# Optimization experiments

Measured on AMD Instinct MI355X. Metric: run time of the kernel, lower is better.

## Reference

```python
import jax, jax.numpy as jnp
import numpy as np

B, L, T = 32, 100, 50
V_SENT, V_FIELD, V_POS = 20000, 1500, 31
E_S, E_F, E_P = 400, 50, 5
FREP = E_F + 2 * E_P            # field rep = field + ppos + pneg embeds
H_DEC = 500                      # decoder hidden
H_DIR = H_DEC // 2               # per-direction encoder hidden
H_ENC = 500                      # encoder_hidden_size (attention/output dim)
IN_ENC = E_S + FREP
EPS = 1e-3


def lstm_cell(x, h, c, Wih, Whh, b):
    z = x @ Wih.T + h @ Whh.T + b
    i, f, g, o = jnp.split(z, 4, axis=-1)
    c = jax.nn.sigmoid(f) * c + jax.nn.sigmoid(i) * jnp.tanh(g)
    h = jax.nn.sigmoid(o) * jnp.tanh(c)
    return h, c


def setup_inputs():
    key = jax.random.key(0)
    ks = jax.random.split(key, 30)
    n = lambda k, sh, s=0.05: jax.random.normal(k, sh, jnp.float32) * s
    return {
        "value_mask": jnp.ones((B, L), jnp.float32),
        "align_prob": jax.random.uniform(ks[0], (B, L, V_SENT), jnp.float32),
        "E_sent": n(ks[1], (V_SENT, E_S)),
        "E_field": n(ks[2], (V_FIELD, E_F)),
        "E_ppos": n(ks[3], (V_POS, E_P)),
        "E_pneg": n(ks[4], (V_POS, E_P)),
        "E_target": n(ks[5], (V_SENT, 300)),
        "enc_Wih_f": n(ks[6], (4 * H_DIR, IN_ENC)),
        "enc_Whh_f": n(ks[7], (4 * H_DIR, H_DIR)),
        "enc_b_f": jnp.zeros((4 * H_DIR,), jnp.float32),
        "enc_Wih_b": n(ks[8], (4 * H_DIR, IN_ENC)),
        "enc_Whh_b": n(ks[9], (4 * H_DIR, H_DIR)),
        "enc_b_b": jnp.zeros((4 * H_DIR,), jnp.float32),
        "dec_Wih": n(ks[10], (4 * H_DEC, E_S)),
        "dec_Whh": n(ks[11], (4 * H_DEC, H_DEC)),
        "dec_b": jnp.zeros((4 * H_DEC,), jnp.float32),
        "W_d": n(ks[12], (H_DEC, H_ENC)),
        "W_z": n(ks[13], (H_DEC, FREP)),
        "W_out": n(ks[14], (H_DEC + H_ENC, H_ENC)),
        "b_out": jnp.zeros((H_ENC,), jnp.float32),
        "w_l": n(ks[15], (H_DEC + H_ENC + E_S, 1)),
        "b_l": jnp.zeros((1,), jnp.float32),
        "W_lin": n(ks[16], (V_SENT, H_ENC)),
        "b_lin": jnp.zeros((V_SENT,), jnp.float32),
        "sent": jax.random.randint(ks[17], (B, T), 0, V_SENT),
        "value": jax.random.randint(ks[18], (B, L), 0, V_SENT),
        "field": jax.random.randint(ks[19], (B, L), 0, V_FIELD),
        "ppos": jax.random.randint(ks[20], (B, L), 0, V_POS),
        "pneg": jax.random.randint(ks[21], (B, L), 0, V_POS),
        "batch_size": B,
    }


def _forward(value_mask, align_prob, E_sent, E_field, E_ppos, E_pneg, E_target,
             enc_Wih_f, enc_Whh_f, enc_b_f, enc_Wih_b, enc_Whh_b, enc_b_b,
             dec_Wih, dec_Whh, dec_b, W_d, W_z, W_out, b_out, w_l, b_l,
             W_lin, b_lin, sent, value, field, ppos, pneg):
    bsz = value.shape[0]
    inp_d = E_sent[value]                                             # [B,L,E_S]
    inp_z = jnp.concatenate([E_field[field], E_ppos[ppos], E_pneg[pneg]], axis=-1)  # [B,L,FREP]
    x = jnp.concatenate([inp_d, inp_z], axis=-1)                      # [B,L,IN_ENC]
    xs = jnp.transpose(x, (1, 0, 2))                                  # [L,B,IN_ENC]
    h0 = jnp.zeros((bsz, H_DIR), x.dtype)

    def enc_step(Wih, Whh, b):
        def f(carry, xt):
            h, c = lstm_cell(xt, carry[0], carry[1], Wih, Whh, b)
            return (h, c), h
        return f

    (hf, cf), hs_f = jax.lax.scan(enc_step(enc_Wih_f, enc_Whh_f, enc_b_f), (h0, h0), xs)
    (hb, cb), hs_b = jax.lax.scan(enc_step(enc_Wih_b, enc_Whh_b, enc_b_b), (h0, h0), xs[::-1])
    enc_out = jnp.transpose(jnp.concatenate([hs_f, hs_b[::-1]], axis=-1), (1, 0, 2))  # [B,L,H_ENC]
    # replicate torch .view on h_n [2,B,H_DIR] -> [B, 2*H_DIR] (row-major, as in source)
    h0_dec = jnp.stack([hf, hb]).reshape(bsz, 2 * H_DIR)
    c0_dec = jnp.stack([cf, cb]).reshape(bsz, 2 * H_DIR)

    sent_emb = jnp.transpose(E_sent[sent], (1, 0, 2))                 # [T,B,E_S]

    def dec_step(carry, xt):
        h, c = lstm_cell(xt, carry[0], carry[1], dec_Wih, dec_Whh, dec_b)
        s_d = jnp.einsum('be,ble->bl', h @ W_d, enc_out)              # attn over encoder states
        s_z = jnp.einsum('bf,blf->bl', h @ W_z, inp_z)                # attn over field reps
        a = jax.nn.softmax(s_d, axis=-1) * jax.nn.softmax(s_z, axis=-1)
        a = a / (jnp.sum(a, axis=-1, keepdims=True) + EPS)            # dual attention
        ctx = jnp.einsum('bl,ble->be', a, enc_out)
        hc = jnp.concatenate([h, ctx], axis=-1)
        out_t = jnp.tanh(hc @ W_out + b_out)                          # [B,H_ENC]
        lam_t = jax.nn.sigmoid(jnp.concatenate([hc, xt], axis=-1) @ w_l + b_l)  # [B,1]
        return (h, c), (out_t, a, lam_t)

    (hT, cT), (outs, attn, lam) = jax.lax.scan(dec_step, (h0_dec, c0_dec), sent_emb)
    outs = jnp.transpose(outs, (1, 0, 2))                             # [B,T,H_ENC]
    attn = jnp.transpose(attn, (1, 0, 2))                             # [B,T,L]
    lam = jnp.transpose(lam, (1, 0, 2))                               # [B,T,1]

    p_mod = jax.nn.log_softmax(outs @ W_lin.T + b_lin, axis=-1)       # [B,T,V]
    p_lex = jnp.einsum('btl,blv->btv', attn, align_prob)              # copy/lexical dist
    p_bias = jax.nn.log_softmax(lam * p_lex + (1.0 - lam) * p_mod, axis=-1)

    # vectorized replacement of the python double-loop position_idx_to_value
    max_idx = jnp.argmax(attn, axis=-1)                               # [B,T]
    word_idx = jnp.take_along_axis(value, max_idx, axis=1)            # [B,T]
    attn_pred = E_target[word_idx]                                    # [B,T,300]
    decoder_pred = E_target[jnp.argmax(p_bias, axis=-1)]              # [B,T,300]
    return p_bias, (hT, cT), attn_pred, decoder_pred


def reference(value_mask, align_prob, E_sent, E_field, E_ppos, E_pneg, E_target,
              enc_Wih_f, enc_Whh_f, enc_b_f, enc_Wih_b, enc_Whh_b, enc_b_b,
              dec_Wih, dec_Whh, dec_b, W_d, W_z, W_out, b_out, w_l, b_l,
              W_lin, b_lin, sent, value, field, ppos, pneg, batch_size):
    return _forward(value_mask, align_prob, E_sent, E_field, E_ppos, E_pneg, E_target,
                    enc_Wih_f, enc_Whh_f, enc_b_f, enc_Wih_b, enc_Whh_b, enc_b_b,
                    dec_Wih, dec_Whh, dec_b, W_d, W_z, W_out, b_out, w_l, b_l,
                    W_lin, b_lin, sent, value, field, ppos, pneg)
```

## Files before the change

kernel.cpp:

```cpp
#include <hip/hip_runtime.h>

#define DI __device__ __forceinline__

constexpr int B = 32, L = 100, T = 50;
constexpr int VS = 20000;
constexpr int HR = 250, HD = 500;
constexpr int INE = 460;
constexpr int OC = 1072;

constexpr size_t O_X      = 0;
constexpr size_t O_SX     = 5888000;
constexpr size_t O_WIHFT  = 8448000;
constexpr size_t O_WIHBT  = 10288000;
constexpr size_t O_WDECT  = 12128000;
constexpr size_t O_W4ENC  = 15328000;
constexpr size_t O_W4DEC  = 17328000;
constexpr size_t O_WCAT   = 21328000;
constexpr size_t O_XWF    = 23472000;
constexpr size_t O_XWB    = 49072000;
constexpr size_t O_XWD    = 74672000;
constexpr size_t O_EOB    = 100272000;
constexpr size_t O_E2     = 113072000;
constexpr size_t O_PROJ   = 125872000;
constexpr size_t O_EHB    = O_PROJ;
constexpr size_t O_DHB    = O_PROJ + 131072;
constexpr size_t O_HD     = 139593600;
constexpr size_t O_H0DEC  = 146249600;
constexpr size_t O_HENCF  = 146505600;
constexpr size_t O_CENCF  = 146633600;
constexpr size_t O_CDEC0  = 146761600;
constexpr size_t O_HDECF  = 146889600;
constexpr size_t O_CDECF  = 147017600;
constexpr size_t O_AD     = 147145600;
constexpr size_t O_ATTN   = 148425600;
constexpr size_t O_EWL    = 149065600;
constexpr size_t O_SXL    = 149091200;
constexpr size_t O_AWL    = 149104000;
constexpr size_t O_LAM    = 149116800;
constexpr size_t O_LS1    = 149123200;
constexpr size_t O_WIDX   = 149129600;
constexpr size_t O_OUTS   = 149144192;
constexpr size_t O_FLG    = 154090496;

constexpr size_t OUT_HT  = 32000000;
constexpr size_t OUT_CT  = 32016000;
constexpr size_t OUT_AP  = 32032000;
constexpr size_t OUT_DP  = 32512000;

DI double dsig(double x) { return 1.0 / (1.0 + exp(-x)); }

DI double cld(const double* p) {
    return __hip_atomic_load(p, __ATOMIC_RELAXED, __HIP_MEMORY_SCOPE_AGENT);
}
DI void cst(double* p, double v) {
    __hip_atomic_store(p, v, __ATOMIC_RELAXED, __HIP_MEMORY_SCOPE_AGENT);
}
DI int cldi(const int* p) {
    return __hip_atomic_load(p, __ATOMIC_RELAXED, __HIP_MEMORY_SCOPE_AGENT);
}
DI void csti(int* p, int v) {
    __hip_atomic_store(p, v, __ATOMIC_RELAXED, __HIP_MEMORY_SCOPE_AGENT);
}
DI void spinge(const int* p, int target) {
    int spins = 0;
    while (cldi(p) < target) {
        __builtin_amdgcn_s_sleep(1);
        if (++spins > 50000000) break;
    }
}


__global__ void k_embed_x(const float* Es, const float* Ef, const float* Ep, const float* En,
                          const int* value, const int* field, const int* ppos, const int* pneg,
                          float* x) {
    int i = blockIdx.x * 256 + threadIdx.x;
    if (i >= B * L * INE) return;
    int j = i % INE, bl = i / INE;
    float v;
    if (j < 400)      v = Es[(size_t)value[bl] * 400 + j];
    else if (j < 450) v = Ef[(size_t)field[bl] * 50 + (j - 400)];
    else if (j < 455) v = Ep[(size_t)ppos[bl] * 5 + (j - 450)];
    else              v = En[(size_t)pneg[bl] * 5 + (j - 455)];
    x[i] = v;
}

__global__ void k_embed_sent(const float* Es, const int* sent, float* sx) {
    int i = blockIdx.x * 256 + threadIdx.x;
    if (i >= T * B * 400) return;
    int k = i % 400, tb = i / 400;
    int b = tb % B, t = tb / B;
    sx[i] = Es[(size_t)sent[b * T + t] * 400 + k];
}

__global__ void k_transpose(float* dst, const float* src, int K, int G) {
    int i = blockIdx.x * 256 + threadIdx.x;
    if (i >= K * G) return;
    int g = i % G, k = i / G;
    dst[i] = src[(size_t)g * K + k];
}

__global__ void k_pack4T(float* dst, const float* src, int U, int Kh) {
    int i = blockIdx.x * 256 + threadIdx.x;
    if (i >= U * Kh * 4) return;
    int g = i & 3, rest = i >> 2;
    int u = rest % U, k = rest / U;
    dst[i] = src[((size_t)(g * U + u)) * Kh + k];
}

__global__ void k_pack_wcat(float* dst, const float* Wd, const float* Wz, const float* Wo, const float* wl) {
    int i = blockIdx.x * 256 + threadIdx.x;
    if (i >= 500 * OC) return;
    int o = i % OC, d = i / OC;
    float v = 0.f;
    if (o < 500)       v = Wd[(size_t)d * 500 + o];
    else if (o < 560)  v = Wz[(size_t)d * 60 + (o - 500)];
    else if (o < 1060) v = Wo[(size_t)d * 500 + (o - 560)];
    else if (o == 1060) v = wl[d];
    dst[i] = v;
}

__global__ void k_zeroi(int* p, int n) {
    int i = blockIdx.x * 256 + threadIdx.x;
    if (i < n) p[i] = 0;
}

__global__ __launch_bounds__(256) void k_gemm_xw(double* out, const float* xs, int bstride, int tstride,
                                                 const float* Wt, const float* bias, int K, int G) {
    __shared__ float xls[460 * 33];
    int t = blockIdx.x;
    int g = blockIdx.y * 256 + threadIdx.x;
    bool act = g < G;
    for (int i = threadIdx.x; i < 32 * K; i += 256) {
        int b = i / K, k = i - b * K;
        xls[k * 33 + b] = xs[(size_t)b * bstride + (size_t)t * tstride + k];
    }
    __syncthreads();
    double acc[32];
    double bs = act ? (double)bias[g] : 0.0;
#pragma unroll
    for (int b = 0; b < 32; ++b) acc[b] = bs;
    for (int k = 0; k < K; ++k) {
        double w = act ? (double)Wt[(size_t)k * G + g] : 0.0;
        const float* xr = &xls[k * 33];
#pragma unroll
        for (int b = 0; b < 32; ++b) acc[b] += w * (double)xr[b];
    }
    if (act) {
#pragma unroll
        for (int b = 0; b < 32; ++b)
            out[((size_t)t * 32 + b) * G + g] = acc[b];
    }
}


__global__ __launch_bounds__(1024) void k_enc_u(const double* xw2F, const double* xw2B,
                                                const float* w4T, double* HB, int* FLG,
                                                double* eoB, double* hencF, double* cencF) {
    __shared__ double h_s[256];
    __shared__ double pz[15][64][4];
    int gid = blockIdx.x;
    int chain = gid >> 2, q = gid & 3;
    int dir = chain >> 5, b = chain & 31;
    int tid = threadIdx.x;
    int kc = tid >> 6, ul = tid & 63;
    int u0 = (q * 250) >> 2, u1 = ((q + 1) * 250) >> 2;
    int nu = u1 - u0;
    int u = u0 + ul;
    bool act = ul < nu;
    int ks = (kc * 250) >> 4, ke = ((kc + 1) * 250) >> 4;
    const double* xw = dir ? xw2B : xw2F;
    const float4* W = (const float4*)w4T + (size_t)dir * 250 * 250;
    double* myHB = HB + (size_t)chain * 256;
    int* flg = FLG + chain * 64;
    double c = 0.0;
    if (tid < 256) h_s[tid] = 0.0;
    __syncthreads();
    for (int s = 0; s < L; ++s) {
        int tin = dir ? (L - 1 - s) : s;
        double zi = 0.0, zf = 0.0, zg = 0.0, zo = 0.0;
        if (act) {
#pragma unroll 4
            for (int k = ks; k < ke; ++k) {
                float4 w = W[(size_t)k * 250 + u];
                double hv = h_s[k];
                zi += (double)w.x * hv; zf += (double)w.y * hv;
                zg += (double)w.z * hv; zo += (double)w.w * hv;
            }
            if (kc) { pz[kc - 1][ul][0] = zi; pz[kc - 1][ul][1] = zf;
                      pz[kc - 1][ul][2] = zg; pz[kc - 1][ul][3] = zo; }
        }
        __syncthreads();
        if (act && kc == 0) {
            const double* x0 = xw + ((size_t)tin * 32 + b) * 1000;
            double Zi = x0[0 * HR + u] + zi, Zf = x0[1 * HR + u] + zf;
            double Zg = x0[2 * HR + u] + zg, Zo = x0[3 * HR + u] + zo;
#pragma unroll
            for (int j = 0; j < 15; ++j) {
                Zi += pz[j][ul][0]; Zf += pz[j][ul][1];
                Zg += pz[j][ul][2]; Zo += pz[j][ul][3];
            }
            double cn = dsig(Zf) * c + dsig(Zi) * tanh(Zg);
            double hn = dsig(Zo) * tanh(cn);
            c = cn;
            cst(&myHB[u], hn);
            eoB[((size_t)b * 100 + tin) * 500 + dir * 250 + u] = hn;
            if (s == L - 1) {
                hencF[dir * 8000 + u * 32 + b] = hn;
                cencF[dir * 8000 + u * 32 + b] = cn;
            }
        }
        __syncthreads();
        if (tid == 0) csti(&flg[q * 16], s + 1);
        if (tid < 4) spinge(&flg[tid * 16], s + 1);
        __syncthreads();
        if (tid < 250) h_s[tid] = cld(&myHB[tid]);
        __syncthreads();
    }
}

__global__ void k_scramble(double* h0dec, double* cdec0, const double* hencF, const double* cencF) {
    int gt = blockIdx.x * 256 + threadIdx.x;
    if (gt >= 16000) return;
    int bb = gt / 500, j = gt - bb * 500;
    int d = gt / 8000, rem = gt - d * 8000;
    int bs = rem / 250, us = rem - bs * 250;
    h0dec[j * 32 + bb] = hencF[d * 8000 + us * 32 + bs];
    cdec0[j * 32 + bb] = cencF[d * 8000 + us * 32 + bs];
}


__global__ __launch_bounds__(1024) void k_dec_u(const double* h0dec, const double* cdec0,
                                                const double* xw2D, const float* w4T,
                                                double* HB, int* FLG,
                                                double* Hd, double* hdecF, double* cdecF) {
    __shared__ double h_s[512];
    __shared__ double pz[15][64][4];
    int gid = blockIdx.x;
    int chain = gid >> 3, q = gid & 7;
    int b = chain;
    int tid = threadIdx.x;
    int kc = tid >> 6, ul = tid & 63;
    int u0 = (q * 500) >> 3, u1 = ((q + 1) * 500) >> 3;
    int nu = u1 - u0;
    int u = u0 + ul;
    bool act = ul < nu;
    int ks = (kc * 500) >> 4, ke = ((kc + 1) * 500) >> 4;
    const float4* W = (const float4*)w4T;
    double* myHB = HB + (size_t)chain * 512;
    int* flg = FLG + chain * 128;
    double c = (act && kc == 0) ? cdec0[u * 32 + b] : 0.0;
    if (tid < 512) h_s[tid] = (tid < 500) ? h0dec[tid * 32 + b] : 0.0;
    __syncthreads();
    for (int t = 0; t < T; ++t) {
        double zi = 0.0, zf = 0.0, zg = 0.0, zo = 0.0;
        if (act) {
#pragma unroll 4
            for (int k = ks; k < ke; ++k) {
                float4 w = W[(size_t)k * 500 + u];
                double hv = h_s[k];
                zi += (double)w.x * hv; zf += (double)w.y * hv;
                zg += (double)w.z * hv; zo += (double)w.w * hv;
            }
            if (kc) { pz[kc - 1][ul][0] = zi; pz[kc - 1][ul][1] = zf;
                      pz[kc - 1][ul][2] = zg; pz[kc - 1][ul][3] = zo; }
        }
        __syncthreads();
        if (act && kc == 0) {
            const double* x0 = xw2D + ((size_t)t * 32 + b) * 2000;
            double Zi = x0[0 * HD + u] + zi, Zf = x0[1 * HD + u] + zf;
            double Zg = x0[2 * HD + u] + zg, Zo = x0[3 * HD + u] + zo;
#pragma unroll
            for (int j = 0; j < 15; ++j) {
                Zi += pz[j][ul][0]; Zf += pz[j][ul][1];
                Zg += pz[j][ul][2]; Zo += pz[j][ul][3];
            }
            double cn = dsig(Zf) * c + dsig(Zi) * tanh(Zg);
            double hn = dsig(Zo) * tanh(cn);
            c = cn;
            cst(&myHB[u], hn);
            Hd[((size_t)t * 32 + b) * 500 + u] = hn;
            if (t == T - 1) {
                hdecF[u * 32 + b] = hn;
                cdecF[u * 32 + b] = cn;
            }
        }
        __syncthreads();
        if (tid == 0) csti(&flg[q * 16], t + 1);
        if (tid < 8) spinge(&flg[tid * 16], t + 1);
        __syncthreads();
        if (tid < 500) h_s[tid] = cld(&myHB[tid]);
        __syncthreads();
    }
}


__global__ __launch_bounds__(256) void k_e2_tiled(const double* eoB, const float* Wo, double* E2) {
    __shared__ double rows[8000];
    int et = blockIdx.x, mt = blockIdx.y;
    int tid = threadIdx.x;
    size_t rbase = (size_t)mt * 16 * 500;
    for (int i = tid; i < 8000; i += 256) rows[i] = eoB[rbase + i];
    __syncthreads();
    int e = et * 256 + tid;
    if (e >= 500) return;
    double acc[16];
#pragma unroll
    for (int m = 0; m < 16; ++m) acc[m] = 0.0;
    for (int d = 0; d < 500; ++d) {
        double w = (double)Wo[(size_t)(500 + d) * 500 + e];
#pragma unroll
        for (int m = 0; m < 16; ++m) acc[m] += rows[m * 500 + d] * w;
    }
#pragma unroll
    for (int m = 0; m < 16; ++m) E2[rbase + (size_t)m * 500 + e] = acc[m];
}

__global__ void k_ewl(const double* eoB, const float* wl, double* E_wl) {
    int w = threadIdx.x >> 6, lane = threadIdx.x & 63;
    int r = blockIdx.x * 4 + w;
    if (r >= 3200) return;
    const double* eo = eoB + (size_t)r * 500;
    double p = 0.0;
    for (int j = lane; j < 500; j += 64) p += eo[j] * (double)wl[500 + j];
    for (int off = 32; off > 0; off >>= 1) p += __shfl_down(p, off);
    if (lane == 0) E_wl[r] = p;
}

__global__ void k_sxl(const float* sx, const float* wl, double* SXL) {
    int i = blockIdx.x * 256 + threadIdx.x;
    if (i >= 1600) return;
    double acc = 0.0;
    for (int k = 0; k < 400; ++k) acc += (double)sx[(size_t)i * 400 + k] * (double)wl[1000 + k];
    SXL[i] = acc;
}

__global__ __launch_bounds__(256) void k_proj_tiled(const double* Hd, const float* Wcat, double* PROJ) {
    __shared__ double rows[8000];
    int ot = blockIdx.x, mt = blockIdx.y;
    int tid = threadIdx.x;
    size_t rbase = (size_t)mt * 16 * 500;
    for (int i = tid; i < 8000; i += 256) rows[i] = Hd[rbase + i];
    __syncthreads();
    int o = ot * 256 + tid;
    if (o >= OC) return;
    double acc[16];
#pragma unroll
    for (int m = 0; m < 16; ++m) acc[m] = 0.0;
    for (int d = 0; d < 500; ++d) {
        double w = (double)Wcat[(size_t)d * OC + o];
#pragma unroll
        for (int m = 0; m < 16; ++m) acc[m] += rows[m * 500 + d] * w;
    }
#pragma unroll
    for (int m = 0; m < 16; ++m)
        PROJ[((size_t)(mt * 16 + m)) * OC + o] = acc[m];
}

__global__ __launch_bounds__(256) void k_attn_all(
        const double* PROJ, const double* eoB, const float* x, const double* E_wl, const int* value,
        float* attn_ws, double* AD, double* AWL, int* widx) {
    int bid = blockIdx.x;
    int t = bid >> 5, b = bid & 31;
    int tid = threadIdx.x;
    int m = b * T + t;
    __shared__ double hwd_s[500], hz_s[60], sd_s[100], sz_s[100], aL[100];
    __shared__ double red[256];
    __shared__ int ri[256];
    const double* pr = PROJ + (size_t)bid * OC;
    for (int k = tid; k < 500; k += 256) hwd_s[k] = pr[k];
    if (tid < 60) hz_s[tid] = pr[500 + tid];
    __syncthreads();
    int w = tid >> 6, lane = tid & 63;
    for (int l = w; l < 100; l += 4) {
        const double* er = eoB + ((size_t)b * 100 + l) * 500;
        double p = 0.0;
        for (int e = lane; e < 500; e += 64) p += hwd_s[e] * er[e];
        for (int off = 32; off > 0; off >>= 1) p += __shfl_down(p, off);
        if (lane == 0) sd_s[l] = p;
        const float* zr = x + ((size_t)b * 100 + l) * 460 + 400;
        double q = (lane < 60) ? hz_s[lane] * (double)zr[lane] : 0.0;
        for (int off = 32; off > 0; off >>= 1) q += __shfl_down(q, off);
        if (lane == 0) sz_s[l] = q;
    }
    __syncthreads();
    red[tid] = (tid < 100) ? sd_s[tid] : -1e300; __syncthreads();
    for (int o = 128; o > 0; o >>= 1) { if (tid < o) red[tid] = fmax(red[tid], red[tid + o]); __syncthreads(); }
    double md = red[0]; __syncthreads();
    red[tid] = (tid < 100) ? exp(sd_s[tid] - md) : 0.0; __syncthreads();
    for (int o = 128; o > 0; o >>= 1) { if (tid < o) red[tid] += red[tid + o]; __syncthreads(); }
    double Sd = red[0]; __syncthreads();
    red[tid] = (tid < 100) ? sz_s[tid] : -1e300; __syncthreads();
    for (int o = 128; o > 0; o >>= 1) { if (tid < o) red[tid] = fmax(red[tid], red[tid + o]); __syncthreads(); }
    double mz = red[0]; __syncthreads();
    red[tid] = (tid < 100) ? exp(sz_s[tid] - mz) : 0.0; __syncthreads();
    for (int o = 128; o > 0; o >>= 1) { if (tid < o) red[tid] += red[tid + o]; __syncthreads(); }
    double Sz = red[0]; __syncthreads();
    if (tid < 100) aL[tid] = (exp(sd_s[tid] - md) / Sd) * (exp(sz_s[tid] - mz) / Sz);
    __syncthreads();
    red[tid] = (tid < 100) ? aL[tid] : 0.0; __syncthreads();
    for (int o = 128; o > 0; o >>= 1) { if (tid < o) red[tid] += red[tid + o]; __syncthreads(); }
    double Sa = red[0]; __syncthreads();
    if (tid < 100) {
        double av = aL[tid] / (Sa + 1e-3);
        aL[tid] = av;
        attn_ws[(size_t)m * 100 + tid] = (float)av;
        AD[(size_t)m * 100 + tid] = av;
    }
    __syncthreads();
    red[tid] = (tid < 100) ? aL[tid] : -1e300;
    ri[tid]  = (tid < 100) ? tid : 0x7fffffff;
    __syncthreads();
    for (int o = 128; o > 0; o >>= 1) {
        if (tid < o) {
            if (red[tid + o] > red[tid] || (red[tid + o] == red[tid] && ri[tid + o] < ri[tid])) {
                red[tid] = red[tid + o]; ri[tid] = ri[tid + o];
            }
        }
        __syncthreads();
    }
    if (tid == 0) widx[m] = value[b * 100 + ri[0]];
    if (tid < 64) {
        double p = (tid < 100) ? aL[tid] * E_wl[b * 100 + tid] : 0.0;
        if (tid + 64 < 100) p += aL[tid + 64] * E_wl[b * 100 + tid + 64];
        for (int off = 32; off > 0; off >>= 1) p += __shfl_down(p, off);
        if (tid == 0) AWL[m] = p;
    }
}

__global__ __launch_bounds__(256) void k_outs(const double* PROJ, const double* AD, const double* E2,
                                              const double* AWL, const double* SXL,
                                              const float* b_out, const float* b_l,
                                              float* outs32, float* lam_ws) {
    __shared__ double ad_s[100];
    int m = blockIdx.x, tid = threadIdx.x;
    int b = m / T, t = m - b * T;
    if (tid < 100) ad_s[tid] = AD[(size_t)m * 100 + tid];
    __syncthreads();
    const double* pr = PROJ + ((size_t)t * 32 + b) * OC;
#pragma unroll 2
    for (int e = tid; e < 512; e += 256) {
        if (e < 500) {
            double acc = pr[560 + e] + (double)b_out[e];
            const double* e2 = E2 + (size_t)b * 50000 + e;
            for (int l = 0; l < 100; ++l) acc += ad_s[l] * e2[l * 500];
            outs32[(size_t)m * 512 + e] = (float)tanh(acc);
        } else {
            outs32[(size_t)m * 512 + e] = 0.f;
        }
    }
    if (tid == 0)
        lam_ws[m] = (float)dsig(pr[1060] + AWL[m] + SXL[t * 32 + b] + (double)b_l[0]);
}

__global__ void k_hTcT(float* out, const double* hdecF, const double* cdecF) {
    int i = blockIdx.x * 256 + threadIdx.x;
    if (i >= 16000) return;
    int b = i / 500, u = i - b * 500;
    out[OUT_HT + i] = (float)hdecF[u * 32 + b];
    out[OUT_CT + i] = (float)cdecF[u * 32 + b];
}


__global__ __launch_bounds__(256) void k_gemm_logits_f32(const float* outs32, const float* W_lin,
                                                         const float* b_lin, float* d_out) {
    __shared__ float As[16][132], Bs[16][132];
    int n0 = blockIdx.x * 128, m0 = blockIdx.y * 128;
    int tid = threadIdx.x;
    int ty = tid >> 4, tx = tid & 15;
    int lr = tid >> 1, lh = tid & 1;
    float acc[8][8];
#pragma unroll
    for (int i = 0; i < 8; ++i)
#pragma unroll
        for (int j = 0; j < 8; ++j) acc[i][j] = 0.f;

    for (int k0 = 0; k0 < 512; k0 += 16) {
        int k8 = k0 + lh * 8;
        float4 a0, a1;
        int mrow = m0 + lr;
        if (mrow < 1600) {
            a0 = *(const float4*)(outs32 + (size_t)mrow * 512 + k8);
            a1 = *(const float4*)(outs32 + (size_t)mrow * 512 + k8 + 4);
        } else {
            a0 = make_float4(0.f, 0.f, 0.f, 0.f); a1 = a0;
        }
        float4 b0 = make_float4(0.f, 0.f, 0.f, 0.f), b1 = b0;
        int nrow = n0 + lr;
        if (nrow < VS) {
            if (k8 < 500)     b0 = *(const float4*)(W_lin + (size_t)nrow * 500 + k8);
            if (k8 + 4 < 500) b1 = *(const float4*)(W_lin + (size_t)nrow * 500 + k8 + 4);
        }
        __syncthreads();
        As[lh * 8 + 0][lr] = a0.x; As[lh * 8 + 1][lr] = a0.y;
        As[lh * 8 + 2][lr] = a0.z; As[lh * 8 + 3][lr] = a0.w;
        As[lh * 8 + 4][lr] = a1.x; As[lh * 8 + 5][lr] = a1.y;
        As[lh * 8 + 6][lr] = a1.z; As[lh * 8 + 7][lr] = a1.w;
        Bs[lh * 8 + 0][lr] = b0.x; Bs[lh * 8 + 1][lr] = b0.y;
        Bs[lh * 8 + 2][lr] = b0.z; Bs[lh * 8 + 3][lr] = b0.w;
        Bs[lh * 8 + 4][lr] = b1.x; Bs[lh * 8 + 5][lr] = b1.y;
        Bs[lh * 8 + 6][lr] = b1.z; Bs[lh * 8 + 7][lr] = b1.w;
        __syncthreads();
#pragma unroll
        for (int kk = 0; kk < 16; ++kk) {
            float4 av0 = *(const float4*)&As[kk][ty * 8];
            float4 av1 = *(const float4*)&As[kk][ty * 8 + 4];
            float4 bv0 = *(const float4*)&Bs[kk][tx * 8];
            float4 bv1 = *(const float4*)&Bs[kk][tx * 8 + 4];
            float ar[8] = {av0.x, av0.y, av0.z, av0.w, av1.x, av1.y, av1.z, av1.w};
            float br[8] = {bv0.x, bv0.y, bv0.z, bv0.w, bv1.x, bv1.y, bv1.z, bv1.w};
#pragma unroll
            for (int i = 0; i < 8; ++i)
#pragma unroll
                for (int j = 0; j < 8; ++j) acc[i][j] += ar[i] * br[j];
        }
    }
#pragma unroll
    for (int j = 0; j < 8; ++j) {
        int n = n0 + tx * 8 + j;
        if (n < VS) {
            float bl = b_lin[n];
#pragma unroll
            for (int i = 0; i < 8; ++i) {
                int mm = m0 + ty * 8 + i;
                if (mm < 1600)
                    d_out[(size_t)mm * VS + n] = acc[i][j] + bl;
            }
        }
    }
}


__global__ void k_red1(const float* d_out, float* LS1) {
    int m = blockIdx.x, tid = threadIdx.x;
    const float* row = d_out + (size_t)m * VS;
    __shared__ float red[256];
    float lm = -3e38f;
    for (int v = tid; v < VS; v += 256) lm = fmaxf(lm, row[v]);
    red[tid] = lm; __syncthreads();
    for (int o = 128; o > 0; o >>= 1) { if (tid < o) red[tid] = fmaxf(red[tid], red[tid + o]); __syncthreads(); }
    float m1 = red[0]; __syncthreads();
    float ls = 0.f;
    for (int v = tid; v < VS; v += 256) ls += expf(row[v] - m1);
    red[tid] = ls; __syncthreads();
    for (int o = 128; o > 0; o >>= 1) { if (tid < o) red[tid] += red[tid + o]; __syncthreads(); }
    if (tid == 0) LS1[m] = m1 + logf(red[0]);
}

__global__ __launch_bounds__(256) void k_plexmix(float* d_out, const float* attn_ws, const float* align_prob,
                                                 const float* lam_ws, const float* LS1) {
    int b = blockIdx.y, v0 = blockIdx.x * 64, tid = threadIdx.x;
    __shared__ float attn_s[50 * 100];
    __shared__ float al[100 * 64];
    for (int i = tid; i < 5000; i += 256) attn_s[i] = attn_ws[(size_t)b * 5000 + i];
    for (int i = tid; i < 6400; i += 256) {
        int l = i >> 6, j = i & 63;
        int v = v0 + j;
        al[i] = (v < VS) ? align_prob[((size_t)b * 100 + l) * VS + v] : 0.f;
    }
    __syncthreads();
    for (int idx = tid; idx < 50 * 64; idx += 256) {
        int t = idx >> 6, j = idx & 63;
        int v = v0 + j;
        if (v < VS) {
            float acc = 0.f;
            for (int l = 0; l < 100; ++l) acc += attn_s[t * 100 + l] * al[l * 64 + j];
            int m = b * T + t;
            size_t p = (size_t)m * VS + v;
            float lamv = lam_ws[m];
            d_out[p] = lamv * acc + (1.f - lamv) * (d_out[p] - LS1[m]);
        }
    }
}

__global__ void k_final2(float* d_out, const float* E_target) {
    int m = blockIdx.x, tid = threadIdx.x;
    float* row = d_out + (size_t)m * VS;
    __shared__ float sm[256], ss[256], sbv[256];
    __shared__ int sbi[256];
    float rm = -3e38f, rs = 0.f, bv = -3e38f; int bi = 0;
    for (int v = tid; v < VS; v += 256) {
        float xv = row[v];
        if (xv > bv) { bv = xv; bi = v; }
        if (xv > rm) { rs = rs * expf(rm - xv) + 1.f; rm = xv; }
        else rs += expf(xv - rm);
    }
    sm[tid] = rm; ss[tid] = rs; sbv[tid] = bv; sbi[tid] = bi;
    __syncthreads();
    for (int o = 128; o > 0; o >>= 1) {
        if (tid < o) {
            float m1 = sm[tid], m2 = sm[tid + o];
            float M = fmaxf(m1, m2);
            ss[tid] = ss[tid] * expf(m1 - M) + ss[tid + o] * expf(m2 - M);
            sm[tid] = M;
            if (sbv[tid + o] > sbv[tid] || (sbv[tid + o] == sbv[tid] && sbi[tid + o] < sbi[tid])) {
                sbv[tid] = sbv[tid + o]; sbi[tid] = sbi[tid + o];
            }
        }
        __syncthreads();
    }
    float ls2 = sm[0] + logf(ss[0]);
    int amax = sbi[0];
    for (int v = tid; v < VS; v += 256) row[v] -= ls2;
    for (int j = tid; j < 300; j += 256)
        d_out[OUT_DP + (size_t)m * 300 + j] = E_target[(size_t)amax * 300 + j];
}

__global__ void k_attnpred2(const int* widx, const float* E_target, float* d_out) {
    int i = blockIdx.x * 256 + threadIdx.x;
    if (i >= 1600 * 300) return;
    int m = i / 300, j = i - m * 300;
    d_out[OUT_AP + i] = E_target[(size_t)widx[m] * 300 + j];
}


extern "C" void kernel_launch(void* const* d_in, const int* in_sizes, int n_in,
                              void* d_out_v, int out_size, void* d_ws, size_t ws_size,
                              hipStream_t stream) {
    const float* align_prob = (const float*)d_in[1];
    const float* E_sent     = (const float*)d_in[2];
    const float* E_field    = (const float*)d_in[3];
    const float* E_ppos     = (const float*)d_in[4];
    const float* E_pneg     = (const float*)d_in[5];
    const float* E_target   = (const float*)d_in[6];
    const float* enc_Wih_f  = (const float*)d_in[7];
    const float* enc_Whh_f  = (const float*)d_in[8];
    const float* enc_b_f    = (const float*)d_in[9];
    const float* enc_Wih_b  = (const float*)d_in[10];
    const float* enc_Whh_b  = (const float*)d_in[11];
    const float* enc_b_b    = (const float*)d_in[12];
    const float* dec_Wih    = (const float*)d_in[13];
    const float* dec_Whh    = (const float*)d_in[14];
    const float* dec_b      = (const float*)d_in[15];
    const float* W_d        = (const float*)d_in[16];
    const float* W_z        = (const float*)d_in[17];
    const float* W_out      = (const float*)d_in[18];
    const float* b_out      = (const float*)d_in[19];
    const float* w_l        = (const float*)d_in[20];
    const float* b_l        = (const float*)d_in[21];
    const float* W_lin      = (const float*)d_in[22];
    const float* b_lin      = (const float*)d_in[23];
    const int* sent  = (const int*)d_in[24];
    const int* value = (const int*)d_in[25];
    const int* field = (const int*)d_in[26];
    const int* ppos  = (const int*)d_in[27];
    const int* pneg  = (const int*)d_in[28];

    char* ws = (char*)d_ws;
    float*  x      = (float*)(ws + O_X);
    float*  sx     = (float*)(ws + O_SX);
    float*  WihfT  = (float*)(ws + O_WIHFT);
    float*  WihbT  = (float*)(ws + O_WIHBT);
    float*  WdecT  = (float*)(ws + O_WDECT);
    float*  w4encT = (float*)(ws + O_W4ENC);
    float*  w4decT = (float*)(ws + O_W4DEC);
    float*  Wcat   = (float*)(ws + O_WCAT);
    double* xwF    = (double*)(ws + O_XWF);
    double* xwB    = (double*)(ws + O_XWB);
    double* xwD    = (double*)(ws + O_XWD);
    double* eoB    = (double*)(ws + O_EOB);
    double* E2     = (double*)(ws + O_E2);
    double* PROJ   = (double*)(ws + O_PROJ);
    double* EHB    = (double*)(ws + O_EHB);
    double* DHB    = (double*)(ws + O_DHB);
    double* Hd     = (double*)(ws + O_HD);
    double* h0dec  = (double*)(ws + O_H0DEC);
    double* hencF  = (double*)(ws + O_HENCF);
    double* cencF  = (double*)(ws + O_CENCF);
    double* cdec0  = (double*)(ws + O_CDEC0);
    double* hdecF  = (double*)(ws + O_HDECF);
    double* cdecF  = (double*)(ws + O_CDECF);
    double* AD     = (double*)(ws + O_AD);
    float*  attn_ws= (float*)(ws + O_ATTN);
    double* E_wl   = (double*)(ws + O_EWL);
    double* SXL    = (double*)(ws + O_SXL);
    double* AWL    = (double*)(ws + O_AWL);
    float*  lam_ws = (float*)(ws + O_LAM);
    float*  LS1    = (float*)(ws + O_LS1);
    int*    widx   = (int*)(ws + O_WIDX);
    float*  outs32 = (float*)(ws + O_OUTS);
    int*    FLGE   = (int*)(ws + O_FLG);
    int*    FLGD   = (int*)(ws + O_FLG) + 8192;
    float* out = (float*)d_out_v;

    k_embed_x<<<(B * L * INE + 255) / 256, 256, 0, stream>>>(E_sent, E_field, E_ppos, E_pneg,
                                                             value, field, ppos, pneg, x);
    k_embed_sent<<<(T * B * 400 + 255) / 256, 256, 0, stream>>>(E_sent, sent, sx);
    k_transpose<<<(460 * 1000 + 255) / 256, 256, 0, stream>>>(WihfT, enc_Wih_f, 460, 1000);
    k_transpose<<<(460 * 1000 + 255) / 256, 256, 0, stream>>>(WihbT, enc_Wih_b, 460, 1000);
    k_transpose<<<(400 * 2000 + 255) / 256, 256, 0, stream>>>(WdecT, dec_Wih, 400, 2000);
    k_pack4T<<<(250 * 250 * 4 + 255) / 256, 256, 0, stream>>>(w4encT, enc_Whh_f, 250, 250);
    k_pack4T<<<(250 * 250 * 4 + 255) / 256, 256, 0, stream>>>(w4encT + 250000, enc_Whh_b, 250, 250);
    k_pack4T<<<(500 * 500 * 4 + 255) / 256, 256, 0, stream>>>(w4decT, dec_Whh, 500, 500);
    k_pack_wcat<<<(500 * OC + 255) / 256, 256, 0, stream>>>(Wcat, W_d, W_z, W_out, w_l);
    k_zeroi<<<(16384 + 255) / 256, 256, 0, stream>>>(FLGE, 16384);
    k_sxl<<<(1600 + 255) / 256, 256, 0, stream>>>(sx, w_l, SXL);
    {
        dim3 g1(100, 4); k_gemm_xw<<<g1, 256, 0, stream>>>(xwF, x, L * INE, INE, WihfT, enc_b_f, 460, 1000);
        dim3 g2(100, 4); k_gemm_xw<<<g2, 256, 0, stream>>>(xwB, x, L * INE, INE, WihbT, enc_b_b, 460, 1000);
        dim3 g3(50, 8);  k_gemm_xw<<<g3, 256, 0, stream>>>(xwD, sx, 400, B * 400, WdecT, dec_b, 400, 2000);
    }

    k_enc_u<<<256, 1024, 0, stream>>>(xwF, xwB, w4encT, EHB, FLGE, eoB, hencF, cencF);
    k_scramble<<<63, 256, 0, stream>>>(h0dec, cdec0, hencF, cencF);
    {
        dim3 ge(2, 200); k_e2_tiled<<<ge, 256, 0, stream>>>(eoB, W_out, E2);
    }
    k_ewl<<<800, 256, 0, stream>>>(eoB, w_l, E_wl);

    k_dec_u<<<256, 1024, 0, stream>>>(h0dec, cdec0, xwD, w4decT, DHB, FLGD, Hd, hdecF, cdecF);
    k_hTcT<<<63, 256, 0, stream>>>(out, hdecF, cdecF);

    {
        dim3 gp(5, 100); k_proj_tiled<<<gp, 256, 0, stream>>>(Hd, Wcat, PROJ);
    }
    k_attn_all<<<1600, 256, 0, stream>>>(PROJ, eoB, x, E_wl, value, attn_ws, AD, AWL, widx);
    k_outs<<<1600, 256, 0, stream>>>(PROJ, AD, E2, AWL, SXL, b_out, b_l, outs32, lam_ws);

    {
        dim3 gg(157, 13);
        k_gemm_logits_f32<<<gg, 256, 0, stream>>>(outs32, W_lin, b_lin, out);
    }
    k_red1<<<1600, 256, 0, stream>>>(out, LS1);
    {
        dim3 gp2(313, 32);
        k_plexmix<<<gp2, 256, 0, stream>>>(out, attn_ws, align_prob, lam_ws, LS1);
    }
    k_final2<<<1600, 256, 0, stream>>>(out, E_target);
    k_attnpred2<<<(1600 * 300 + 255) / 256, 256, 0, stream>>>(widx, E_target, out);
}
```

Baseline: 3.178 ms.

## Switch post-recurrence attention/projection pipeline from fp64 to fp32 and fix pz layout

Converts the encoder/decoder outputs and all downstream attention, projection, E2 and output kernels from double to float storage and arithmetic. The recurrent LSTM cells themselves stay in double. It also transposes the shared partial-sum array so lanes access consecutive addresses, which reduces LDS bank conflicts. The aim is to cut fp64 ALU cost and memory traffic in the non-recurrent stages, at the price of lower precision in the attention and argmax selection.

```diff
diff --git a/kernel.cpp b/kernel.cpp
--- a/kernel.cpp
+++ b/kernel.cpp
@@ -48,6 +48,7 @@
 constexpr size_t OUT_DP  = 32512000;
 
 DI double dsig(double x) { return 1.0 / (1.0 + exp(-x)); }
+DI float fsig(float x) { return 1.f / (1.f + expf(-x)); }
 
 DI double cld(const double* p) {
     return __hip_atomic_load(p, __ATOMIC_RELAXED, __HIP_MEMORY_SCOPE_AGENT);
@@ -155,9 +156,9 @@
 
 __global__ __launch_bounds__(1024) void k_enc_u(const double* xw2F, const double* xw2B,
                                                 const float* w4T, double* HB, int* FLG,
-                                                double* eoB, double* hencF, double* cencF) {
+                                                float* eoB, double* hencF, double* cencF) {
     __shared__ double h_s[256];
-    __shared__ double pz[15][64][4];
+    __shared__ double pz[15][4][64];
     int gid = blockIdx.x;
     int chain = gid >> 2, q = gid & 3;
     int dir = chain >> 5, b = chain & 31;
@@ -186,8 +187,8 @@
                 zi += (double)w.x * hv; zf += (double)w.y * hv;
                 zg += (double)w.z * hv; zo += (double)w.w * hv;
             }
-            if (kc) { pz[kc - 1][ul][0] = zi; pz[kc - 1][ul][1] = zf;
-                      pz[kc - 1][ul][2] = zg; pz[kc - 1][ul][3] = zo; }
+            if (kc) { pz[kc - 1][0][ul] = zi; pz[kc - 1][1][ul] = zf;
+                      pz[kc - 1][2][ul] = zg; pz[kc - 1][3][ul] = zo; }
         }
         __syncthreads();
         if (act && kc == 0) {
@@ -196,14 +197,14 @@
             double Zg = x0[2 * HR + u] + zg, Zo = x0[3 * HR + u] + zo;
 #pragma unroll
             for (int j = 0; j < 15; ++j) {
-                Zi += pz[j][ul][0]; Zf += pz[j][ul][1];
-                Zg += pz[j][ul][2]; Zo += pz[j][ul][3];
+                Zi += pz[j][0][ul]; Zf += pz[j][1][ul];
+                Zg += pz[j][2][ul]; Zo += pz[j][3][ul];
             }
             double cn = dsig(Zf) * c + dsig(Zi) * tanh(Zg);
             double hn = dsig(Zo) * tanh(cn);
             c = cn;
             cst(&myHB[u], hn);
-            eoB[((size_t)b * 100 + tin) * 500 + dir * 250 + u] = hn;
+            eoB[((size_t)b * 100 + tin) * 500 + dir * 250 + u] = (float)hn;
             if (s == L - 1) {
                 hencF[dir * 8000 + u * 32 + b] = hn;
                 cencF[dir * 8000 + u * 32 + b] = cn;
@@ -232,9 +233,9 @@
 __global__ __launch_bounds__(1024) void k_dec_u(const double* h0dec, const double* cdec0,
                                                 const double* xw2D, const float* w4T,
                                                 double* HB, int* FLG,
-                                                double* Hd, double* hdecF, double* cdecF) {
+                                                float* Hd, double* hdecF, double* cdecF) {
     __shared__ double h_s[512];
-    __shared__ double pz[15][64][4];
+    __shared__ double pz[15][4][64];
     int gid = blockIdx.x;
     int chain = gid >> 3, q = gid & 7;
     int b = chain;
@@ -261,8 +262,8 @@
                 zi += (double)w.x * hv; zf += (double)w.y * hv;
                 zg += (double)w.z * hv; zo += (double)w.w * hv;
             }
-            if (kc) { pz[kc - 1][ul][0] = zi; pz[kc - 1][ul][1] = zf;
-                      pz[kc - 1][ul][2] = zg; pz[kc - 1][ul][3] = zo; }
+            if (kc) { pz[kc - 1][0][ul] = zi; pz[kc - 1][1][ul] = zf;
+                      pz[kc - 1][2][ul] = zg; pz[kc - 1][3][ul] = zo; }
         }
         __syncthreads();
         if (act && kc == 0) {
@@ -271,14 +272,14 @@
             double Zg = x0[2 * HD + u] + zg, Zo = x0[3 * HD + u] + zo;
 #pragma unroll
             for (int j = 0; j < 15; ++j) {
-                Zi += pz[j][ul][0]; Zf += pz[j][ul][1];
-                Zg += pz[j][ul][2]; Zo += pz[j][ul][3];
+                Zi += pz[j][0][ul]; Zf += pz[j][1][ul];
+                Zg += pz[j][2][ul]; Zo += pz[j][3][ul];
             }
             double cn = dsig(Zf) * c + dsig(Zi) * tanh(Zg);
             double hn = dsig(Zo) * tanh(cn);
             c = cn;
             cst(&myHB[u], hn);
-            Hd[((size_t)t * 32 + b) * 500 + u] = hn;
+            Hd[((size_t)t * 32 + b) * 500 + u] = (float)hn;
             if (t == T - 1) {
                 hdecF[u * 32 + b] = hn;
                 cdecF[u * 32 + b] = cn;
@@ -294,8 +295,8 @@
 }
 
 
-__global__ __launch_bounds__(256) void k_e2_tiled(const double* eoB, const float* Wo, double* E2) {
-    __shared__ double rows[8000];
+__global__ __launch_bounds__(256) void k_e2_tiled(const float* eoB, const float* Wo, float* E2) {
+    __shared__ float rows[8000];
     int et = blockIdx.x, mt = blockIdx.y;
     int tid = threadIdx.x;
     size_t rbase = (size_t)mt * 16 * 500;
@@ -303,11 +304,11 @@
     __syncthreads();
     int e = et * 256 + tid;
     if (e >= 500) return;
-    double acc[16];
-#pragma unroll
-    for (int m = 0; m < 16; ++m) acc[m] = 0.0;
+    float acc[16];
+#pragma unroll
+    for (int m = 0; m < 16; ++m) acc[m] = 0.f;
     for (int d = 0; d < 500; ++d) {
-        double w = (double)Wo[(size_t)(500 + d) * 500 + e];
+        float w = Wo[(size_t)(500 + d) * 500 + e];
 #pragma unroll
         for (int m = 0; m < 16; ++m) acc[m] += rows[m * 500 + d] * w;
     }
@@ -315,27 +316,27 @@
     for (int m = 0; m < 16; ++m) E2[rbase + (size_t)m * 500 + e] = acc[m];
 }
 
-__global__ void k_ewl(const double* eoB, const float* wl, double* E_wl) {
+__global__ void k_ewl(const float* eoB, const float* wl, float* E_wl) {
     int w = threadIdx.x >> 6, lane = threadIdx.x & 63;
     int r = blockIdx.x * 4 + w;
     if (r >= 3200) return;
-    const double* eo = eoB + (size_t)r * 500;
-    double p = 0.0;
-    for (int j = lane; j < 500; j += 64) p += eo[j] * (double)wl[500 + j];
+    const float* eo = eoB + (size_t)r * 500;
+    float p = 0.f;
+    for (int j = lane; j < 500; j += 64) p += eo[j] * wl[500 + j];
     for (int off = 32; off > 0; off >>= 1) p += __shfl_down(p, off);
     if (lane == 0) E_wl[r] = p;
 }
 
-__global__ void k_sxl(const float* sx, const float* wl, double* SXL) {
+__global__ void k_sxl(const float* sx, const float* wl, float* SXL) {
     int i = blockIdx.x * 256 + threadIdx.x;
     if (i >= 1600) return;
-    double acc = 0.0;
-    for (int k = 0; k < 400; ++k) acc += (double)sx[(size_t)i * 400 + k] * (double)wl[1000 + k];
+    float acc = 0.f;
+    for (int k = 0; k < 400; ++k) acc += sx[(size_t)i * 400 + k] * wl[1000 + k];
     SXL[i] = acc;
 }
 
-__global__ __launch_bounds__(256) void k_proj_tiled(const double* Hd, const float* Wcat, double* PROJ) {
-    __shared__ double rows[8000];
+__global__ __launch_bounds__(256) void k_proj_tiled(const float* Hd, const float* Wcat, float* PROJ) {
+    __shared__ float rows[8000];
     int ot = blockIdx.x, mt = blockIdx.y;
     int tid = threadIdx.x;
     size_t rbase = (size_t)mt * 16 * 500;
@@ -343,11 +344,11 @@
     __syncthreads();
     int o = ot * 256 + tid;
     if (o >= OC) return;
-    double acc[16];
-#pragma unroll
-    for (int m = 0; m < 16; ++m) acc[m] = 0.0;
+    float acc[16];
+#pragma unroll
+    for (int m = 0; m < 16; ++m) acc[m] = 0.f;
     for (int d = 0; d < 500; ++d) {
-        double w = (double)Wcat[(size_t)d * OC + o];
+        float w = Wcat[(size_t)d * OC + o];
 #pragma unroll
         for (int m = 0; m < 16; ++m) acc[m] += rows[m * 500 + d] * w;
     }
@@ -357,57 +358,57 @@
 }
 
 __global__ __launch_bounds__(256) void k_attn_all(
-        const double* PROJ, const double* eoB, const float* x, const double* E_wl, const int* value,
-        float* attn_ws, double* AD, double* AWL, int* widx) {
+        const float* PROJ, const float* eoB, const float* x, const float* E_wl, const int* value,
+        float* attn_ws, float* AD, float* AWL, int* widx) {
     int bid = blockIdx.x;
     int t = bid >> 5, b = bid & 31;
     int tid = threadIdx.x;
     int m = b * T + t;
-    __shared__ double hwd_s[500], hz_s[60], sd_s[100], sz_s[100], aL[100];
-    __shared__ double red[256];
+    __shared__ float hwd_s[500], hz_s[60], sd_s[100], sz_s[100], aL[100];
+    __shared__ float red[256];
     __shared__ int ri[256];
-    const double* pr = PROJ + (size_t)bid * OC;
+    const float* pr = PROJ + (size_t)bid * OC;
     for (int k = tid; k < 500; k += 256) hwd_s[k] = pr[k];
     if (tid < 60) hz_s[tid] = pr[500 + tid];
     __syncthreads();
     int w = tid >> 6, lane = tid & 63;
     for (int l = w; l < 100; l += 4) {
-        const double* er = eoB + ((size_t)b * 100 + l) * 500;
-        double p = 0.0;
+        const float* er = eoB + ((size_t)b * 100 + l) * 500;
+        float p = 0.f;
         for (int e = lane; e < 500; e += 64) p += hwd_s[e] * er[e];
         for (int off = 32; off > 0; off >>= 1) p += __shfl_down(p, off);
         if (lane == 0) sd_s[l] = p;
         const float* zr = x + ((size_t)b * 100 + l) * 460 + 400;
-        double q = (lane < 60) ? hz_s[lane] * (double)zr[lane] : 0.0;
-        for (int off = 32; off > 0; off >>= 1) q += __shfl_down(q, off);
-        if (lane == 0) sz_s[l] = q;
-    }
-    __syncthreads();
-    red[tid] = (tid < 100) ? sd_s[tid] : -1e300; __syncthreads();
-    for (int o = 128; o > 0; o >>= 1) { if (tid < o) red[tid] = fmax(red[tid], red[tid + o]); __syncthreads(); }
-    double md = red[0]; __syncthreads();
-    red[tid] = (tid < 100) ? exp(sd_s[tid] - md) : 0.0; __syncthreads();
+        float qq = (lane < 60) ? hz_s[lane] * zr[lane] : 0.f;
+        for (int off = 32; off > 0; off >>= 1) qq += __shfl_down(qq, off);
+        if (lane == 0) sz_s[l] = qq;
+    }
+    __syncthreads();
+    red[tid] = (tid < 100) ? sd_s[tid] : -3e38f; __syncthreads();
+    for (int o = 128; o > 0; o >>= 1) { if (tid < o) red[tid] = fmaxf(red[tid], red[tid + o]); __syncthreads(); }
+    float md = red[0]; __syncthreads();
+    red[tid] = (tid < 100) ? expf(sd_s[tid] - md) : 0.f; __syncthreads();
     for (int o = 128; o > 0; o >>= 1) { if (tid < o) red[tid] += red[tid + o]; __syncthreads(); }
-    double Sd = red[0]; __syncthreads();
-    red[tid] = (tid < 100) ? sz_s[tid] : -1e300; __syncthreads();
-    for (int o = 128; o > 0; o >>= 1) { if (tid < o) red[tid] = fmax(red[tid], red[tid + o]); __syncthreads(); }
-    double mz = red[0]; __syncthreads();
-    red[tid] = (tid < 100) ? exp(sz_s[tid] - mz) : 0.0; __syncthreads();
+    float Sd = red[0]; __syncthreads();
+    red[tid] = (tid < 100) ? sz_s[tid] : -3e38f; __syncthreads();
+    for (int o = 128; o > 0; o >>= 1) { if (tid < o) red[tid] = fmaxf(red[tid], red[tid + o]); __syncthreads(); }
+    float mz = red[0]; __syncthreads();
+    red[tid] = (tid < 100) ? expf(sz_s[tid] - mz) : 0.f; __syncthreads();
     for (int o = 128; o > 0; o >>= 1) { if (tid < o) red[tid] += red[tid + o]; __syncthreads(); }
-    double Sz = red[0]; __syncthreads();
-    if (tid < 100) aL[tid] = (exp(sd_s[tid] - md) / Sd) * (exp(sz_s[tid] - mz) / Sz);
-    __syncthreads();
-    red[tid] = (tid < 100) ? aL[tid] : 0.0; __syncthreads();
+    float Sz = red[0]; __syncthreads();
+    if (tid < 100) aL[tid] = (expf(sd_s[tid] - md) / Sd) * (expf(sz_s[tid] - mz) / Sz);
+    __syncthreads();
+    red[tid] = (tid < 100) ? aL[tid] : 0.f; __syncthreads();
     for (int o = 128; o > 0; o >>= 1) { if (tid < o) red[tid] += red[tid + o]; __syncthreads(); }
-    double Sa = red[0]; __syncthreads();
+    float Sa = red[0]; __syncthreads();
     if (tid < 100) {
-        double av = aL[tid] / (Sa + 1e-3);
+        float av = aL[tid] / (Sa + 1e-3f);
         aL[tid] = av;
-        attn_ws[(size_t)m * 100 + tid] = (float)av;
+        attn_ws[(size_t)m * 100 + tid] = av;
         AD[(size_t)m * 100 + tid] = av;
     }
     __syncthreads();
-    red[tid] = (tid < 100) ? aL[tid] : -1e300;
+    red[tid] = (tid < 100) ? aL[tid] : -3e38f;
     ri[tid]  = (tid < 100) ? tid : 0x7fffffff;
     __syncthreads();
     for (int o = 128; o > 0; o >>= 1) {
@@ -420,36 +421,36 @@
     }
     if (tid == 0) widx[m] = value[b * 100 + ri[0]];
     if (tid < 64) {
-        double p = (tid < 100) ? aL[tid] * E_wl[b * 100 + tid] : 0.0;
+        float p = (tid < 100) ? aL[tid] * E_wl[b * 100 + tid] : 0.f;
         if (tid + 64 < 100) p += aL[tid + 64] * E_wl[b * 100 + tid + 64];
         for (int off = 32; off > 0; off >>= 1) p += __shfl_down(p, off);
         if (tid == 0) AWL[m] = p;
     }
 }
 
-__global__ __launch_bounds__(256) void k_outs(const double* PROJ, const double* AD, const double* E2,
-                                              const double* AWL, const double* SXL,
+__global__ __launch_bounds__(256) void k_outs(const float* PROJ, const float* AD, const float* E2,
+                                              const float* AWL, const float* SXL,
                                               const float* b_out, const float* b_l,
                                               float* outs32, float* lam_ws) {
-    __shared__ double ad_s[100];
+    __shared__ float ad_s[100];
     int m = blockIdx.x, tid = threadIdx.x;
     int b = m / T, t = m - b * T;
     if (tid < 100) ad_s[tid] = AD[(size_t)m * 100 + tid];
     __syncthreads();
-    const double* pr = PROJ + ((size_t)t * 32 + b) * OC;
+    const float* pr = PROJ + ((size_t)t * 32 + b) * OC;
 #pragma unroll 2
     for (int e = tid; e < 512; e += 256) {
         if (e < 500) {
-            double acc = pr[560 + e] + (double)b_out[e];
-            const double* e2 = E2 + (size_t)b * 50000 + e;
+            float acc = pr[560 + e] + b_out[e];
+            const float* e2 = E2 + (size_t)b * 50000 + e;
             for (int l = 0; l < 100; ++l) acc += ad_s[l] * e2[l * 500];
-            outs32[(size_t)m * 512 + e] = (float)tanh(acc);
+            outs32[(size_t)m * 512 + e] = tanhf(acc);
         } else {
             outs32[(size_t)m * 512 + e] = 0.f;
         }
     }
     if (tid == 0)
-        lam_ws[m] = (float)dsig(pr[1060] + AWL[m] + SXL[t * 32 + b] + (double)b_l[0]);
+        lam_ws[m] = fsig(pr[1060] + AWL[m] + SXL[t * 32 + b] + b_l[0]);
 }
 
 __global__ void k_hTcT(float* out, const double* hdecF, const double* cdecF) {
@@ -657,23 +658,23 @@
     double* xwF    = (double*)(ws + O_XWF);
     double* xwB    = (double*)(ws + O_XWB);
     double* xwD    = (double*)(ws + O_XWD);
-    double* eoB    = (double*)(ws + O_EOB);
-    double* E2     = (double*)(ws + O_E2);
-    double* PROJ   = (double*)(ws + O_PROJ);
+    float*  eoB    = (float*)(ws + O_EOB);
+    float*  E2     = (float*)(ws + O_E2);
+    float*  PROJ   = (float*)(ws + O_PROJ);
     double* EHB    = (double*)(ws + O_EHB);
     double* DHB    = (double*)(ws + O_DHB);
-    double* Hd     = (double*)(ws + O_HD);
+    float*  Hd     = (float*)(ws + O_HD);
     double* h0dec  = (double*)(ws + O_H0DEC);
     double* hencF  = (double*)(ws + O_HENCF);
     double* cencF  = (double*)(ws + O_CENCF);
     double* cdec0  = (double*)(ws + O_CDEC0);
     double* hdecF  = (double*)(ws + O_HDECF);
     double* cdecF  = (double*)(ws + O_CDECF);
-    double* AD     = (double*)(ws + O_AD);
+    float*  AD     = (float*)(ws + O_AD);
     float*  attn_ws= (float*)(ws + O_ATTN);
-    double* E_wl   = (double*)(ws + O_EWL);
-    double* SXL    = (double*)(ws + O_SXL);
-    double* AWL    = (double*)(ws + O_AWL);
+    float*  E_wl   = (float*)(ws + O_EWL);
+    float*  SXL    = (float*)(ws + O_SXL);
+    float*  AWL    = (float*)(ws + O_AWL);
     float*  lam_ws = (float*)(ws + O_LAM);
     float*  LS1    = (float*)(ws + O_LS1);
     int*    widx   = (int*)(ws + O_WIDX);
```

Result: faster. 3.040 ms, median of 2 (-4.4%).
